# Kernel optimization log

Measured on AMD Instinct MI355X. Metric: run time of the kernel, lower is better.

Reference implementation:

```python
import jax, jax.numpy as jnp
import numpy as np
import hashlib

MAX_HASH_VALUE = 2 ** 8  # 256
BATCH, MAX_LEN, EMB, HID, VOCAB = 32, 512, 256, 1024, 32000


def _hash_mod(flat_ids, algo):
    # SHA digest interpreted little-endian; only value mod 256 matters for the
    # downstream (h1 + k*h2) % 256, and mod 256 of a little-endian int is just
    # the first digest byte. We keep the full int.from_bytes for faithfulness.
    return np.array(
        [int.from_bytes(algo(str(int(v)).encode()).digest(), 'little') % MAX_HASH_VALUE
         for v in flat_ids],
        dtype=np.int64,
    )


def setup_inputs() -> dict:
    key = jax.random.key(0)
    k1, k2, k3 = jax.random.split(key, 3)
    input_ids = jax.random.randint(k1, (BATCH, MAX_LEN), 0, VOCAB, dtype=jnp.int64)
    W = jax.random.normal(k2, (HID, EMB), dtype=jnp.float32) * (1.0 / np.sqrt(EMB))
    b = jax.random.normal(k3, (HID,), dtype=jnp.float32) * 0.01
    return {"input_ids": input_ids, "W": W, "b": b}


def reference(input_ids, W, b):
    ids = np.asarray(input_ids)            # [B, L] int
    B, L = ids.shape
    flat = ids.reshape(-1)
    h1 = _hash_mod(flat, hashlib.sha256).reshape(B, L)   # [B, L] in [0,256)
    h2 = _hash_mod(flat, hashlib.sha224).reshape(B, L)
    k = jnp.arange(EMB, dtype=jnp.int64)                 # [E]
    # hash3[b,l,k] = (h1 + k*h2) % 256
    hash3 = ((jnp.asarray(h1)[:, :, None] + k[None, None, :] * jnp.asarray(h2)[:, :, None])
             % MAX_HASH_VALUE).astype(jnp.float32)        # [B, L, E]
    out = jnp.einsum('ble,he->blh', hash3, W) + b        # [B, L, H]
    return out
```

## Files before the change

### kernel.cpp

```cpp
#include <hip/hip_runtime.h>
#include <stdint.h>

typedef short bf16x8 __attribute__((ext_vector_type(8)));
typedef float f32x16 __attribute__((ext_vector_type(16)));
typedef unsigned short ushort_t;

#define EMB 256
#define HID 1024
#define NTOK 16384

#define WS_W_OFF 0

#define ROTR(x,n) (((x)>>(n))|((x)<<(32-(n))))
#define S0F(x) (ROTR((x),7)^ROTR((x),18)^((x)>>3))
#define S1F(x) (ROTR((x),17)^ROTR((x),19)^((x)>>10))

#define RND1(Kc, Wt) do {                                                          \
    uint32_t t1_ = sh + (ROTR(se,6)^ROTR(se,11)^ROTR(se,25))                       \
                   + ((se&sf)^(~se&sg)) + (Kc) + (Wt);                             \
    uint32_t t2_ = (ROTR(sa,2)^ROTR(sa,13)^ROTR(sa,22))                            \
                   + ((sa&sb)^(sa&sc)^(sb&sc));                                    \
    sh=sg; sg=sf; sf=se; se=sd+t1_; sd=sc; sc=sb; sb=sa; sa=t1_+t2_; } while (0)

#define WSXS(a,b,c,d) ((a) += S0F(b) + (c) + S1F(d))

__device__ __forceinline__ uint32_t rbf(float x) {
    uint32_t b = __float_as_uint(x);
    return (b + 0x7FFFu + ((b >> 16) & 1u)) >> 16;
}
__device__ __forceinline__ uint4 pack8(float4 a, float4 b) {
    uint4 q;
    q.x = rbf(a.x) | (rbf(a.y) << 16);
    q.y = rbf(a.z) | (rbf(a.w) << 16);
    q.z = rbf(b.x) | (rbf(b.y) << 16);
    q.w = rbf(b.z) | (rbf(b.w) << 16);
    return q;
}

#define MFMA(av,bv,acc) __builtin_amdgcn_mfma_f32_32x32x16_bf16(av,bv,acc,0,0,0)

__global__ __launch_bounds__(256) void prep_kernel(const float* __restrict__ W,
                                                   ushort_t* __restrict__ Wf) {
    const int t = blockIdx.x * 256 + threadIdx.x;
    const int h = t >> 4;
    const int kk = t & 15;
    const float4* wsrc = reinterpret_cast<const float4*>(W + h * EMB + kk * 16);
    float4 a = wsrc[0], b = wsrc[1], c = wsrc[2], d = wsrc[3];
    uint4 qa = pack8(a, b);
    uint4 qb = pack8(c, d);
    uint4* wbase = reinterpret_cast<uint4*>(Wf) + ((size_t)(h >> 5) * 16 + kk) * 64 + (h & 31);
    wbase[0]  = qa;
    wbase[32] = qb;
}

__global__ __launch_bounds__(256, 2) void fused_kernel(const uint32_t* __restrict__ ids32,
                                                       const ushort_t* __restrict__ Wf,
                                                       const float* __restrict__ bias,
                                                       float* __restrict__ out) {
    __shared__ uint4 Albuf[4096];
    __shared__ uint32_t redf[4];

    const int bid = blockIdx.x;
    const int bm = bid >> 2;
    const int nb0 = (bid & 3) * 256;
    const int tid = (int)threadIdx.x;
    const int wv = tid >> 6, lane = tid & 63, lrow = lane & 31, lh = lane >> 5;
    const int wm = wv >> 1, wn = wv & 1;

    {
        const uint4* ids4 = reinterpret_cast<const uint4*>(ids32);
        uint4 da = ids4[tid], db = ids4[tid + 256];
        uint32_t z = da.y | da.w | db.y | db.w;
        unsigned long long m = __ballot(z != 0u);
        if (lane == 0) redf[wv] = (m != 0ull) ? 1u : 0u;
    }
    __syncthreads();
    const bool is64 = (redf[0] | redf[1] | redf[2] | redf[3]) == 0u;

    const int rr = tid >> 1;
    const uint32_t st = tid & 1;
    const int tok = bm * 128 + rr;
    const uint32_t v = is64 ? ids32[2 * tok] : ids32[tok];

    const uint32_t q4 = __umulhi(v, 0xD1B71759u) >> 13;
    const uint32_t r4 = v - q4 * 10000u;
    const uint32_t q3 = __umulhi(r4, 0x10624DD3u) >> 6;
    const uint32_t r3 = r4 - q3 * 1000u;
    const uint32_t q2 = __umulhi(r3, 0x51EB851Fu) >> 5;
    const uint32_t r2 = r3 - q2 * 100u;
    const uint32_t q1 = __umulhi(r2, 0xCCCCCCCDu) >> 3;
    const uint32_t q0 = r2 - q1 * 10u;
    const uint32_t nd = v >= 10000u ? 5u : v >= 1000u ? 4u : v >= 100u ? 3u
                         : v >= 10u ? 2u : 1u;
    uint64_t M = ((uint64_t)(q4 + '0') << 56) | ((uint64_t)(q3 + '0') << 48) |
                 ((uint64_t)(q2 + '0') << 40) | ((uint64_t)(q1 + '0') << 32) |
                 ((uint64_t)(q0 + '0') << 24) | ((uint64_t)0x80u << 16);
    M <<= 8u * (5u - nd);

    uint32_t w0 = (uint32_t)(M >> 32), w1 = (uint32_t)M;
    uint32_t w2 = 0, w3 = 0, w4 = 0, w5 = 0, w6 = 0, w7 = 0;
    uint32_t w8 = 0, w9 = 0, w10 = 0, w11 = 0, w12 = 0, w13 = 0, w14 = 0;
    uint32_t w15 = nd * 8u;

    uint32_t sa = st ? 0xc1059ed8u : 0x6a09e667u;
    uint32_t sb = st ? 0x367cd507u : 0xbb67ae85u;
    uint32_t sc = st ? 0x3070dd17u : 0x3c6ef372u;
    uint32_t sd = st ? 0xf70e5939u : 0xa54ff53au;
    uint32_t se = st ? 0xffc00b31u : 0x510e527fu;
    uint32_t sf = st ? 0x68581511u : 0x9b05688cu;
    uint32_t sg = st ? 0x64f98fa7u : 0x1f83d9abu;
    uint32_t sh = st ? 0xbefa4fa4u : 0x5be0cd19u;

    RND1(0x428a2f98u, w0);  RND1(0x71374491u, w1);  RND1(0xb5c0fbcfu, w2);
    RND1(0xe9b5dba5u, w3);  RND1(0x3956c25bu, w4);  RND1(0x59f111f1u, w5);
    RND1(0x923f82a4u, w6);  RND1(0xab1c5ed5u, w7);  RND1(0xd807aa98u, w8);
    RND1(0x12835b01u, w9);  RND1(0x243185beu, w10); RND1(0x550c7dc3u, w11);
    RND1(0x72be5d74u, w12); RND1(0x80deb1feu, w13); RND1(0x9bdc06a7u, w14);
    RND1(0xc19bf174u, w15);
    WSXS(w0,w1,w9,w14);    RND1(0xe49b69c1u, w0);
    WSXS(w1,w2,w10,w15);   RND1(0xefbe4786u, w1);
    WSXS(w2,w3,w11,w0);    RND1(0x0fc19dc6u, w2);
    WSXS(w3,w4,w12,w1);    RND1(0x240ca1ccu, w3);
    WSXS(w4,w5,w13,w2);    RND1(0x2de92c6fu, w4);
    WSXS(w5,w6,w14,w3);    RND1(0x4a7484aau, w5);
    WSXS(w6,w7,w15,w4);    RND1(0x5cb0a9dcu, w6);
    WSXS(w7,w8,w0,w5);     RND1(0x76f988dau, w7);
    WSXS(w8,w9,w1,w6);     RND1(0x983e5152u, w8);
    WSXS(w9,w10,w2,w7);    RND1(0xa831c66du, w9);
    WSXS(w10,w11,w3,w8);   RND1(0xb00327c8u, w10);
    WSXS(w11,w12,w4,w9);   RND1(0xbf597fc7u, w11);
    WSXS(w12,w13,w5,w10);  RND1(0xc6e00bf3u, w12);
    WSXS(w13,w14,w6,w11);  RND1(0xd5a79147u, w13);
    WSXS(w14,w15,w7,w12);  RND1(0x06ca6351u, w14);
    WSXS(w15,w0,w8,w13);   RND1(0x14292967u, w15);
    WSXS(w0,w1,w9,w14);    RND1(0x27b70a85u, w0);
    WSXS(w1,w2,w10,w15);   RND1(0x2e1b2138u, w1);
    WSXS(w2,w3,w11,w0);    RND1(0x4d2c6dfcu, w2);
    WSXS(w3,w4,w12,w1);    RND1(0x53380d13u, w3);
    WSXS(w4,w5,w13,w2);    RND1(0x650a7354u, w4);
    WSXS(w5,w6,w14,w3);    RND1(0x766a0abbu, w5);
    WSXS(w6,w7,w15,w4);    RND1(0x81c2c92eu, w6);
    WSXS(w7,w8,w0,w5);     RND1(0x92722c85u, w7);
    WSXS(w8,w9,w1,w6);     RND1(0xa2bfe8a1u, w8);
    WSXS(w9,w10,w2,w7);    RND1(0xa81a664bu, w9);
    WSXS(w10,w11,w3,w8);   RND1(0xc24b8b70u, w10);
    WSXS(w11,w12,w4,w9);   RND1(0xc76c51a3u, w11);
    WSXS(w12,w13,w5,w10);  RND1(0xd192e819u, w12);
    WSXS(w13,w14,w6,w11);  RND1(0xd6990624u, w13);
    WSXS(w14,w15,w7,w12);  RND1(0xf40e3585u, w14);
    WSXS(w15,w0,w8,w13);   RND1(0x106aa070u, w15);
    WSXS(w0,w1,w9,w14);    RND1(0x19a4c116u, w0);
    WSXS(w1,w2,w10,w15);   RND1(0x1e376c08u, w1);
    WSXS(w2,w3,w11,w0);    RND1(0x2748774cu, w2);
    WSXS(w3,w4,w12,w1);    RND1(0x34b0bcb5u, w3);
    WSXS(w4,w5,w13,w2);    RND1(0x391c0cb3u, w4);
    WSXS(w5,w6,w14,w3);    RND1(0x4ed8aa4au, w5);
    WSXS(w6,w7,w15,w4);    RND1(0x5b9cca4fu, w6);
    WSXS(w7,w8,w0,w5);     RND1(0x682e6ff3u, w7);
    WSXS(w8,w9,w1,w6);     RND1(0x748f82eeu, w8);
    WSXS(w9,w10,w2,w7);    RND1(0x78a5636fu, w9);
    WSXS(w10,w11,w3,w8);   RND1(0x84c87814u, w10);
    WSXS(w11,w12,w4,w9);   RND1(0x8cc70208u, w11);
    WSXS(w12,w13,w5,w10);  RND1(0x90befffau, w12);
    WSXS(w13,w14,w6,w11);  RND1(0xa4506cebu, w13);
    WSXS(w14,w15,w7,w12);  RND1(0xbef9a3f7u, w14);
    WSXS(w15,w0,w8,w13);   RND1(0xc67178f2u, w15);

    const uint32_t hv = ((st ? 0xc1059ed8u : 0x6a09e667u) + sa) >> 24;
    const uint32_t hvo = __shfl_xor(hv, 1);
    const uint32_t hv1 = st ? hvo : hv;
    const uint32_t hv2 = st ? hv : hvo;

    {
        const int ag = rr >> 5, aslot = rr & 31;
        uint32_t val = (hv1 + (st ? ((hv2 << 7) & 255u) : 0u)) & 255u;
        const int kfb = (int)st * 8;
#define PAIR(dst) { uint32_t lo_ = val; uint32_t hi_ = (val + hv2) & 255u;        \
                    val = (hi_ + hv2) & 255u;                                     \
                    dst = (__float_as_uint((float)lo_) >> 16) |                   \
                          (__float_as_uint((float)hi_) & 0xFFFF0000u); }
#pragma unroll
        for (int q = 0; q < 8; ++q) {
            uint32_t c0_, c1_, c2_, c3_, c4_, c5_, c6_, c7_;
            PAIR(c0_); PAIR(c1_); PAIR(c2_); PAIR(c3_);
            PAIR(c4_); PAIR(c5_); PAIR(c6_); PAIR(c7_);
            uint4 qa; qa.x = c0_; qa.y = c1_; qa.z = c2_; qa.w = c3_;
            uint4 qb; qb.x = c4_; qb.y = c5_; qb.z = c6_; qb.w = c7_;
            Albuf[(ag * 16 + kfb + q) * 64 + aslot]      = qa;
            Albuf[(ag * 16 + kfb + q) * 64 + aslot + 32] = qb;
        }
#undef PAIR
    }

    const int cb = nb0 + wn * 64 + lrow;
    const float bs00 = bias[cb],       bs01 = bias[cb + 32];
    const float bs10 = bias[cb + 128], bs11 = bias[cb + 160];

    __syncthreads();

    const bf16x8* bfr = reinterpret_cast<const bf16x8*>(Wf);
    const bf16x8* alr = reinterpret_cast<const bf16x8*>(Albuf);
    const int agA0 = (wm * 2) * 16, agA1 = (wm * 2 + 1) * 16;
    const int m0 = bm * 128 + wm * 64;

#define DO_SUB(sub, bj0_, bj1_) do {                                               \
    const int gb0_ = (nb0 >> 5) + (sub) * 4 + wn * 2;                              \
    f32x16 a00 = (f32x16)(0.0f), a01 = (f32x16)(0.0f);                             \
    f32x16 a10 = (f32x16)(0.0f), a11 = (f32x16)(0.0f);                             \
    _Pragma("unroll 2")                                                            \
    for (int kf = 0; kf < 16; ++kf) {                                              \
        bf16x8 bv0 = bfr[((size_t)(gb0_ * 16 + kf)) * 64 + lane];                  \
        bf16x8 bv1 = bfr[((size_t)((gb0_ + 1) * 16 + kf)) * 64 + lane];            \
        bf16x8 av0 = alr[(agA0 + kf) * 64 + lane];                                 \
        bf16x8 av1 = alr[(agA1 + kf) * 64 + lane];                                 \
        a00 = MFMA(av0, bv0, a00); a01 = MFMA(av0, bv1, a01);                      \
        a10 = MFMA(av1, bv0, a10); a11 = MFMA(av1, bv1, a11);                      \
    }                                                                              \
    const int col_ = nb0 + (sub) * 128 + wn * 64 + lrow;                           \
    _Pragma("unroll")                                                              \
    for (int r_ = 0; r_ < 16; ++r_) {                                              \
        const int rowl_ = (r_ & 3) + 8 * (r_ >> 2) + 4 * lh;                       \
        const size_t o0_ = (size_t)(m0 + rowl_) * HID + col_;                      \
        const size_t o1_ = o0_ + (size_t)32 * HID;                                 \
        __builtin_nontemporal_store(a00[r_] + bj0_, &out[o0_]);                    \
        __builtin_nontemporal_store(a01[r_] + bj1_, &out[o0_ + 32]);               \
        __builtin_nontemporal_store(a10[r_] + bj0_, &out[o1_]);                    \
        __builtin_nontemporal_store(a11[r_] + bj1_, &out[o1_ + 32]);               \
    } } while (0)

    DO_SUB(0, bs00, bs01);
    DO_SUB(1, bs10, bs11);

#undef DO_SUB
}

extern "C" void kernel_launch(void* const* d_in, const int* in_sizes, int n_in,
                              void* d_out, int out_size, void* d_ws, size_t ws_size,
                              hipStream_t stream) {
    const uint32_t* ids32 = (const uint32_t*)d_in[0];
    const float* W = (const float*)d_in[1];
    const float* bias = (const float*)d_in[2];
    float* out = (float*)d_out;
    ushort_t* Wf = (ushort_t*)((char*)d_ws + WS_W_OFF);
    (void)in_sizes; (void)n_in; (void)out_size; (void)ws_size;

    prep_kernel<<<64, 256, 0, stream>>>(W, Wf);
    fused_kernel<<<512, 256, 0, stream>>>(ids32, Wf, bias, out);
}
```

Measured before the change: 34.98 us.

## Move SHA hashing into prep kernel and shrink GEMM tiles to 64 rows

```diff
diff --git a/kernel.cpp b/kernel.cpp
--- a/kernel.cpp
+++ b/kernel.cpp
@@ -10,6 +10,7 @@
 #define NTOK 16384
 
 #define WS_W_OFF 0
+#define WS_H_OFF (512u * 1024u)
 
 #define ROTR(x,n) (((x)>>(n))|((x)<<(32-(n))))
 #define S0F(x) (ROTR((x),7)^ROTR((x),18)^((x)>>3))
@@ -39,47 +40,30 @@
 
 #define MFMA(av,bv,acc) __builtin_amdgcn_mfma_f32_32x32x16_bf16(av,bv,acc,0,0,0)
 
-__global__ __launch_bounds__(256) void prep_kernel(const float* __restrict__ W,
-                                                   ushort_t* __restrict__ Wf) {
-    const int t = blockIdx.x * 256 + threadIdx.x;
-    const int h = t >> 4;
-    const int kk = t & 15;
-    const float4* wsrc = reinterpret_cast<const float4*>(W + h * EMB + kk * 16);
-    float4 a = wsrc[0], b = wsrc[1], c = wsrc[2], d = wsrc[3];
-    uint4 qa = pack8(a, b);
-    uint4 qb = pack8(c, d);
-    uint4* wbase = reinterpret_cast<uint4*>(Wf) + ((size_t)(h >> 5) * 16 + kk) * 64 + (h & 31);
-    wbase[0]  = qa;
-    wbase[32] = qb;
-}
-
-__global__ __launch_bounds__(256, 2) void fused_kernel(const uint32_t* __restrict__ ids32,
-                                                       const ushort_t* __restrict__ Wf,
-                                                       const float* __restrict__ bias,
-                                                       float* __restrict__ out) {
-    __shared__ uint4 Albuf[4096];
-    __shared__ uint32_t redf[4];
-
-    const int bid = blockIdx.x;
-    const int bm = bid >> 2;
-    const int nb0 = (bid & 3) * 256;
+__global__ __launch_bounds__(128) void prep_kernel(const uint32_t* __restrict__ ids32,
+                                                   const float* __restrict__ W,
+                                                   ushort_t* __restrict__ Wf,
+                                                   ushort_t* __restrict__ Hs) {
+    __shared__ uint32_t redf[2];
     const int tid = (int)threadIdx.x;
-    const int wv = tid >> 6, lane = tid & 63, lrow = lane & 31, lh = lane >> 5;
-    const int wm = wv >> 1, wn = wv & 1;
+    const int g = (int)blockIdx.x * 128 + tid;
+
+    const int h = g >> 5, c8 = g & 31, kk = c8 >> 1, h8 = c8 & 1;
+    const float4* wsrc = reinterpret_cast<const float4*>(W + h * EMB + kk * 16 + h8 * 8);
+    float4 wa = wsrc[0], wb = wsrc[1];
 
     {
         const uint4* ids4 = reinterpret_cast<const uint4*>(ids32);
-        uint4 da = ids4[tid], db = ids4[tid + 256];
+        uint4 da = ids4[tid], db = ids4[tid + 128];
         uint32_t z = da.y | da.w | db.y | db.w;
         unsigned long long m = __ballot(z != 0u);
-        if (lane == 0) redf[wv] = (m != 0ull) ? 1u : 0u;
+        if ((tid & 63) == 0) redf[tid >> 6] = (m != 0ull) ? 1u : 0u;
     }
     __syncthreads();
-    const bool is64 = (redf[0] | redf[1] | redf[2] | redf[3]) == 0u;
-
-    const int rr = tid >> 1;
-    const uint32_t st = tid & 1;
-    const int tok = bm * 128 + rr;
+    const bool is64 = (redf[0] | redf[1]) == 0u;
+
+    const int tok = g >> 1;
+    const uint32_t st = g & 1;
     const uint32_t v = is64 ? ids32[2 * tok] : ids32[tok];
 
     const uint32_t q4 = __umulhi(v, 0xD1B71759u) >> 13;
@@ -168,70 +152,87 @@
 
     const uint32_t hv = ((st ? 0xc1059ed8u : 0x6a09e667u) + sa) >> 24;
     const uint32_t hvo = __shfl_xor(hv, 1);
-    const uint32_t hv1 = st ? hvo : hv;
-    const uint32_t hv2 = st ? hv : hvo;
+    if (st == 0) Hs[tok] = (ushort_t)(hv | (hvo << 8));
+
+    uint4* wbase = reinterpret_cast<uint4*>(Wf) + ((size_t)(h >> 5) * 16 + kk) * 64
+                   + (h & 31) + h8 * 32;
+    *wbase = pack8(wa, wb);
+}
+
+__global__ __launch_bounds__(256, 4) void fused_kernel(const ushort_t* __restrict__ Hs,
+                                                       const ushort_t* __restrict__ Wf,
+                                                       const float* __restrict__ bias,
+                                                       float* __restrict__ out) {
+    __shared__ uint4 Albuf[2048];
+
+    const int bid = blockIdx.x;
+    const int bm = bid >> 2;
+    const int nb0 = (bid & 3) * 256;
+    const int tid = (int)threadIdx.x;
+    const int wv = tid >> 6, lane = tid & 63, lrow = lane & 31, lh = lane >> 5;
+    const int wn2 = wv >> 1;
+    const int ga = wv & 1;
 
     {
-        const int ag = rr >> 5, aslot = rr & 31;
-        uint32_t val = (hv1 + (st ? ((hv2 << 7) & 255u) : 0u)) & 255u;
-        const int kfb = (int)st * 8;
+        const int tk = tid >> 2;
+        const int g4 = tid & 3;
+        const uint32_t hsv = Hs[bm * 64 + tk];
+        const uint32_t hv1 = hsv & 255u, hv2 = hsv >> 8;
+        const int ag = tk >> 5, aslot = tk & 31;
+        const int kf0 = g4 * 4;
+        uint32_t val = (hv1 + hv2 * (uint32_t)(g4 << 6)) & 255u;
 #define PAIR(dst) { uint32_t lo_ = val; uint32_t hi_ = (val + hv2) & 255u;        \
                     val = (hi_ + hv2) & 255u;                                     \
                     dst = (__float_as_uint((float)lo_) >> 16) |                   \
                           (__float_as_uint((float)hi_) & 0xFFFF0000u); }
 #pragma unroll
-        for (int q = 0; q < 8; ++q) {
+        for (int q = 0; q < 4; ++q) {
             uint32_t c0_, c1_, c2_, c3_, c4_, c5_, c6_, c7_;
             PAIR(c0_); PAIR(c1_); PAIR(c2_); PAIR(c3_);
             PAIR(c4_); PAIR(c5_); PAIR(c6_); PAIR(c7_);
             uint4 qa; qa.x = c0_; qa.y = c1_; qa.z = c2_; qa.w = c3_;
             uint4 qb; qb.x = c4_; qb.y = c5_; qb.z = c6_; qb.w = c7_;
-            Albuf[(ag * 16 + kfb + q) * 64 + aslot]      = qa;
-            Albuf[(ag * 16 + kfb + q) * 64 + aslot + 32] = qb;
+            Albuf[(ag * 0 + (tk >> 5) * 16 + kf0 + q) * 64 + aslot]      = qa;
+            Albuf[((tk >> 5) * 16 + kf0 + q) * 64 + aslot + 32]          = qb;
         }
 #undef PAIR
     }
 
-    const int cb = nb0 + wn * 64 + lrow;
-    const float bs00 = bias[cb],       bs01 = bias[cb + 32];
-    const float bs10 = bias[cb + 128], bs11 = bias[cb + 160];
+    const int cb = nb0 + wn2 * 128 + lrow;
+    const float bj0 = bias[cb], bj1 = bias[cb + 32];
+    const float bj2 = bias[cb + 64], bj3 = bias[cb + 96];
 
     __syncthreads();
 
     const bf16x8* bfr = reinterpret_cast<const bf16x8*>(Wf);
     const bf16x8* alr = reinterpret_cast<const bf16x8*>(Albuf);
-    const int agA0 = (wm * 2) * 16, agA1 = (wm * 2 + 1) * 16;
-    const int m0 = bm * 128 + wm * 64;
-
-#define DO_SUB(sub, bj0_, bj1_) do {                                               \
-    const int gb0_ = (nb0 >> 5) + (sub) * 4 + wn * 2;                              \
-    f32x16 a00 = (f32x16)(0.0f), a01 = (f32x16)(0.0f);                             \
-    f32x16 a10 = (f32x16)(0.0f), a11 = (f32x16)(0.0f);                             \
-    _Pragma("unroll 2")                                                            \
-    for (int kf = 0; kf < 16; ++kf) {                                              \
-        bf16x8 bv0 = bfr[((size_t)(gb0_ * 16 + kf)) * 64 + lane];                  \
-        bf16x8 bv1 = bfr[((size_t)((gb0_ + 1) * 16 + kf)) * 64 + lane];            \
-        bf16x8 av0 = alr[(agA0 + kf) * 64 + lane];                                 \
-        bf16x8 av1 = alr[(agA1 + kf) * 64 + lane];                                 \
-        a00 = MFMA(av0, bv0, a00); a01 = MFMA(av0, bv1, a01);                      \
-        a10 = MFMA(av1, bv0, a10); a11 = MFMA(av1, bv1, a11);                      \
-    }                                                                              \
-    const int col_ = nb0 + (sub) * 128 + wn * 64 + lrow;                           \
-    _Pragma("unroll")                                                              \
-    for (int r_ = 0; r_ < 16; ++r_) {                                              \
-        const int rowl_ = (r_ & 3) + 8 * (r_ >> 2) + 4 * lh;                       \
-        const size_t o0_ = (size_t)(m0 + rowl_) * HID + col_;                      \
-        const size_t o1_ = o0_ + (size_t)32 * HID;                                 \
-        __builtin_nontemporal_store(a00[r_] + bj0_, &out[o0_]);                    \
-        __builtin_nontemporal_store(a01[r_] + bj1_, &out[o0_ + 32]);               \
-        __builtin_nontemporal_store(a10[r_] + bj0_, &out[o1_]);                    \
-        __builtin_nontemporal_store(a11[r_] + bj1_, &out[o1_ + 32]);               \
-    } } while (0)
-
-    DO_SUB(0, bs00, bs01);
-    DO_SUB(1, bs10, bs11);
-
-#undef DO_SUB
+    const int gb0 = (nb0 >> 5) + wn2 * 4;
+    const int agA = ga * 16;
+
+    f32x16 a0 = (f32x16)(0.0f), a1 = (f32x16)(0.0f);
+    f32x16 a2 = (f32x16)(0.0f), a3 = (f32x16)(0.0f);
+
+#pragma unroll 2
+    for (int kf = 0; kf < 16; ++kf) {
+        bf16x8 av  = alr[(agA + kf) * 64 + lane];
+        bf16x8 bv0 = bfr[((size_t)((gb0 + 0) * 16 + kf)) * 64 + lane];
+        bf16x8 bv1 = bfr[((size_t)((gb0 + 1) * 16 + kf)) * 64 + lane];
+        bf16x8 bv2 = bfr[((size_t)((gb0 + 2) * 16 + kf)) * 64 + lane];
+        bf16x8 bv3 = bfr[((size_t)((gb0 + 3) * 16 + kf)) * 64 + lane];
+        a0 = MFMA(av, bv0, a0); a1 = MFMA(av, bv1, a1);
+        a2 = MFMA(av, bv2, a2); a3 = MFMA(av, bv3, a3);
+    }
+
+    const int m0 = bm * 64 + ga * 32;
+#pragma unroll
+    for (int r = 0; r < 16; ++r) {
+        const int rowl = (r & 3) + 8 * (r >> 2) + 4 * lh;
+        const size_t o = (size_t)(m0 + rowl) * HID + cb;
+        __builtin_nontemporal_store(a0[r] + bj0, &out[o]);
+        __builtin_nontemporal_store(a1[r] + bj1, &out[o + 32]);
+        __builtin_nontemporal_store(a2[r] + bj2, &out[o + 64]);
+        __builtin_nontemporal_store(a3[r] + bj3, &out[o + 96]);
+    }
 }
 
 extern "C" void kernel_launch(void* const* d_in, const int* in_sizes, int n_in,
@@ -242,8 +243,9 @@
     const float* bias = (const float*)d_in[2];
     float* out = (float*)d_out;
     ushort_t* Wf = (ushort_t*)((char*)d_ws + WS_W_OFF);
+    ushort_t* Hs = (ushort_t*)((char*)d_ws + WS_H_OFF);
     (void)in_sizes; (void)n_in; (void)out_size; (void)ws_size;
 
-    prep_kernel<<<64, 256, 0, stream>>>(W, Wf);
-    fused_kernel<<<512, 256, 0, stream>>>(ids32, Wf, bias, out);
-}
+    prep_kernel<<<256, 128, 0, stream>>>(ids32, W, Wf, Hs);
+    fused_kernel<<<1024, 256, 0, stream>>>(Hs, Wf, bias, out);
+}
```

Measured after the change: 42.74 us. 1.22x slower.

## Permute W columns so each lane stores contiguous float4 output vectors

Applied to the files above, without the earlier changes.

```diff
diff --git a/kernel.cpp b/kernel.cpp
--- a/kernel.cpp
+++ b/kernel.cpp
@@ -3,6 +3,7 @@
 
 typedef short bf16x8 __attribute__((ext_vector_type(8)));
 typedef float f32x16 __attribute__((ext_vector_type(16)));
+typedef float f32x4 __attribute__((ext_vector_type(4)));
 typedef unsigned short ushort_t;
 
 #define EMB 256
@@ -39,18 +40,18 @@
 
 #define MFMA(av,bv,acc) __builtin_amdgcn_mfma_f32_32x32x16_bf16(av,bv,acc,0,0,0)
 
-__global__ __launch_bounds__(256) void prep_kernel(const float* __restrict__ W,
-                                                   ushort_t* __restrict__ Wf) {
-    const int t = blockIdx.x * 256 + threadIdx.x;
+__global__ __launch_bounds__(64) void prep_kernel(const float* __restrict__ W,
+                                                  ushort_t* __restrict__ Wf) {
+    const int t = (int)blockIdx.x * 64 + (int)threadIdx.x;
     const int h = t >> 4;
     const int kk = t & 15;
     const float4* wsrc = reinterpret_cast<const float4*>(W + h * EMB + kk * 16);
     float4 a = wsrc[0], b = wsrc[1], c = wsrc[2], d = wsrc[3];
-    uint4 qa = pack8(a, b);
-    uint4 qb = pack8(c, d);
-    uint4* wbase = reinterpret_cast<uint4*>(Wf) + ((size_t)(h >> 5) * 16 + kk) * 64 + (h & 31);
-    wbase[0]  = qa;
-    wbase[32] = qb;
+    const int P = h >> 7, hl = h & 127, j = hl & 3, cc = hl >> 2;
+    uint4* wbase = reinterpret_cast<uint4*>(Wf)
+                   + ((size_t)(P * 4 + j) * 16 + kk) * 64 + cc;
+    wbase[0]  = pack8(a, b);
+    wbase[32] = pack8(c, d);
 }
 
 __global__ __launch_bounds__(256, 2) void fused_kernel(const uint32_t* __restrict__ ids32,
@@ -65,7 +66,8 @@
     const int nb0 = (bid & 3) * 256;
     const int tid = (int)threadIdx.x;
     const int wv = tid >> 6, lane = tid & 63, lrow = lane & 31, lh = lane >> 5;
-    const int wm = wv >> 1, wn = wv & 1;
+    const int wm = wv >> 1;
+    const int wn2 = wv & 1;
 
     {
         const uint4* ids4 = reinterpret_cast<const uint4*>(ids32);
@@ -192,46 +194,50 @@
 #undef PAIR
     }
 
-    const int cb = nb0 + wn * 64 + lrow;
-    const float bs00 = bias[cb],       bs01 = bias[cb + 32];
-    const float bs10 = bias[cb + 128], bs11 = bias[cb + 160];
+    const int C0 = nb0 + wn2 * 128;
+    const f32x4 b4 = *reinterpret_cast<const f32x4*>(bias + C0 + 4 * lrow);
 
     __syncthreads();
 
     const bf16x8* bfr = reinterpret_cast<const bf16x8*>(Wf);
     const bf16x8* alr = reinterpret_cast<const bf16x8*>(Albuf);
+    const int gb0 = (C0 >> 7) * 4;
     const int agA0 = (wm * 2) * 16, agA1 = (wm * 2 + 1) * 16;
+
+    f32x16 A00 = (f32x16)(0.0f), A01 = (f32x16)(0.0f);
+    f32x16 A02 = (f32x16)(0.0f), A03 = (f32x16)(0.0f);
+    f32x16 A10 = (f32x16)(0.0f), A11 = (f32x16)(0.0f);
+    f32x16 A12 = (f32x16)(0.0f), A13 = (f32x16)(0.0f);
+
+#pragma unroll 2
+    for (int kf = 0; kf < 16; ++kf) {
+        bf16x8 av0 = alr[(agA0 + kf) * 64 + lane];
+        bf16x8 av1 = alr[(agA1 + kf) * 64 + lane];
+        bf16x8 bv0 = bfr[((size_t)((gb0 + 0) * 16 + kf)) * 64 + lane];
+        bf16x8 bv1 = bfr[((size_t)((gb0 + 1) * 16 + kf)) * 64 + lane];
+        bf16x8 bv2 = bfr[((size_t)((gb0 + 2) * 16 + kf)) * 64 + lane];
+        bf16x8 bv3 = bfr[((size_t)((gb0 + 3) * 16 + kf)) * 64 + lane];
+        A00 = MFMA(av0, bv0, A00); A01 = MFMA(av0, bv1, A01);
+        A02 = MFMA(av0, bv2, A02); A03 = MFMA(av0, bv3, A03);
+        A10 = MFMA(av1, bv0, A10); A11 = MFMA(av1, bv1, A11);
+        A12 = MFMA(av1, bv2, A12); A13 = MFMA(av1, bv3, A13);
+    }
+
     const int m0 = bm * 128 + wm * 64;
-
-#define DO_SUB(sub, bj0_, bj1_) do {                                               \
-    const int gb0_ = (nb0 >> 5) + (sub) * 4 + wn * 2;                              \
-    f32x16 a00 = (f32x16)(0.0f), a01 = (f32x16)(0.0f);                             \
-    f32x16 a10 = (f32x16)(0.0f), a11 = (f32x16)(0.0f);                             \
-    _Pragma("unroll 2")                                                            \
-    for (int kf = 0; kf < 16; ++kf) {                                              \
-        bf16x8 bv0 = bfr[((size_t)(gb0_ * 16 + kf)) * 64 + lane];                  \
-        bf16x8 bv1 = bfr[((size_t)((gb0_ + 1) * 16 + kf)) * 64 + lane];            \
-        bf16x8 av0 = alr[(agA0 + kf) * 64 + lane];                                 \
-        bf16x8 av1 = alr[(agA1 + kf) * 64 + lane];                                 \
-        a00 = MFMA(av0, bv0, a00); a01 = MFMA(av0, bv1, a01);                      \
-        a10 = MFMA(av1, bv0, a10); a11 = MFMA(av1, bv1, a11);                      \
-    }                                                                              \
-    const int col_ = nb0 + (sub) * 128 + wn * 64 + lrow;                           \
-    _Pragma("unroll")                                                              \
-    for (int r_ = 0; r_ < 16; ++r_) {                                              \
-        const int rowl_ = (r_ & 3) + 8 * (r_ >> 2) + 4 * lh;                       \
-        const size_t o0_ = (size_t)(m0 + rowl_) * HID + col_;                      \
-        const size_t o1_ = o0_ + (size_t)32 * HID;                                 \
-        __builtin_nontemporal_store(a00[r_] + bj0_, &out[o0_]);                    \
-        __builtin_nontemporal_store(a01[r_] + bj1_, &out[o0_ + 32]);               \
-        __builtin_nontemporal_store(a10[r_] + bj0_, &out[o1_]);                    \
-        __builtin_nontemporal_store(a11[r_] + bj1_, &out[o1_ + 32]);               \
-    } } while (0)
-
-    DO_SUB(0, bs00, bs01);
-    DO_SUB(1, bs10, bs11);
-
-#undef DO_SUB
+    float* obase = out + (size_t)C0 + 4 * lrow;
+#pragma unroll
+    for (int r = 0; r < 16; ++r) {
+        const int rowl = (r & 3) + 8 * (r >> 2) + 4 * lh;
+        f32x4 v0, v1;
+        v0[0] = A00[r] + b4[0]; v0[1] = A01[r] + b4[1];
+        v0[2] = A02[r] + b4[2]; v0[3] = A03[r] + b4[3];
+        v1[0] = A10[r] + b4[0]; v1[1] = A11[r] + b4[1];
+        v1[2] = A12[r] + b4[2]; v1[3] = A13[r] + b4[3];
+        __builtin_nontemporal_store(
+            v0, reinterpret_cast<f32x4*>(obase + (size_t)(m0 + rowl) * HID));
+        __builtin_nontemporal_store(
+            v1, reinterpret_cast<f32x4*>(obase + (size_t)(m0 + 32 + rowl) * HID));
+    }
 }
 
 extern "C" void kernel_launch(void* const* d_in, const int* in_sizes, int n_in,
@@ -244,6 +250,6 @@
     ushort_t* Wf = (ushort_t*)((char*)d_ws + WS_W_OFF);
     (void)in_sizes; (void)n_in; (void)out_size; (void)ws_size;
 
-    prep_kernel<<<64, 256, 0, stream>>>(W, Wf);
+    prep_kernel<<<256, 64, 0, stream>>>(W, Wf);
     fused_kernel<<<512, 256, 0, stream>>>(ids32, Wf, bias, out);
 }
```

Result: no change. 35.32 us (+1.0%).
